# Kernel tuning notes

Hardware: AMD Instinct MI355X
Metric: run time of the kernel (lower is better)

Reference implementation:

```python
import jax, jax.numpy as jnp
import numpy as np

B, N, C, M = 1, 384, 128, 128
EPS = 1e-5

def _ln(x, g, b):
    mu = jnp.mean(x, axis=-1, keepdims=True)
    var = jnp.mean(jnp.square(x - mu), axis=-1, keepdims=True)
    return (x - mu) * jax.lax.rsqrt(var + EPS) * g + b

def setup_inputs() -> dict:
    key = jax.random.key(0)
    ks = jax.random.split(key, 12)
    s = 0.02
    return {
        "act": jax.random.normal(ks[0], (B, N, N, C), dtype=jnp.float32),
        "mask": jnp.ones((B, N, N), dtype=jnp.float32),
        "ln_g": jnp.ones((C,), jnp.float32), "ln_b": jnp.zeros((C,), jnp.float32),
        "Wl": s * jax.random.normal(ks[1], (C, M)), "bl": jnp.zeros((M,)),
        "Wr": s * jax.random.normal(ks[2], (C, M)), "br": jnp.zeros((M,)),
        "Wgl": s * jax.random.normal(ks[3], (C, M)), "bgl": jnp.zeros((M,)),
        "Wgr": s * jax.random.normal(ks[4], (C, M)), "bgr": jnp.zeros((M,)),
        "cg": jnp.ones((M,), jnp.float32), "cb": jnp.zeros((M,), jnp.float32),
        "Wo": s * jax.random.normal(ks[5], (M, C)), "bo": jnp.zeros((C,)),
        "Wg": s * jax.random.normal(ks[6], (C, C)), "bg": jnp.zeros((C,)),
    }

def reference(act, mask, ln_g, ln_b, Wl, bl, Wr, br, Wgl, bgl, Wgr, bgr, cg, cb, Wo, bo, Wg, bg):
    x = _ln(act, ln_g, ln_b)                      # [B,N,N,C]
    m = mask[..., None]                           # [B,N,N,1]
    left = m * (x @ Wl + bl) * jax.nn.sigmoid(x @ Wgl + bgl)   # [B,N,N,M]
    right = m * (x @ Wr + br) * jax.nn.sigmoid(x @ Wgr + bgr)  # [B,N,N,M]
    gate = jax.nn.sigmoid(x @ Wg + bg)            # [B,N,N,C]
    out = jnp.einsum('bikc,bjkc->bijc', left, right)  # triangle contraction over k
    out = _ln(out, cg, cb)
    out = (out @ Wo + bo) * gate
    return out
```

## Files before the change

kernel.cpp:

```cpp
#include <hip/hip_runtime.h>

#define EPS 1e-5f
#define NDIM 384
#define CDIM 128
#define NN (NDIM * NDIM)

typedef unsigned short ushort_t;
typedef __attribute__((ext_vector_type(8))) short short8;
typedef __attribute__((ext_vector_type(4))) float floatx4;
typedef __attribute__((ext_vector_type(4))) unsigned int uint4v;
typedef __attribute__((ext_vector_type(4))) float float4v;

static __device__ __forceinline__ ushort_t f2bf(float f) {
    unsigned int u = __builtin_bit_cast(unsigned int, f);
    u += 0x7FFFu + ((u >> 16) & 1u);
    return (ushort_t)(u >> 16);
}
static __device__ __forceinline__ float bf2f(ushort_t h) {
    unsigned int u = ((unsigned int)h) << 16;
    return __builtin_bit_cast(float, u);
}
static __device__ __forceinline__ float sigmoidf_(float x) {
    return 1.0f / (1.0f + __expf(-x));
}
static __device__ __forceinline__ floatx4 mfma16(short8 a, short8 b, floatx4 c) {
    return __builtin_amdgcn_mfma_f32_16x16x32_bf16(a, b, c, 0, 0, 0);
}

__global__ __launch_bounds__(256) void wconv6(
    const float* __restrict__ Wl, const float* __restrict__ Wr,
    const float* __restrict__ Wgl, const float* __restrict__ Wgr,
    const float* __restrict__ Wg, const float* __restrict__ Wo,
    ushort_t* __restrict__ wt)
{
    __shared__ float tile[128 * 132];
    const float* Ws[6] = {Wl, Wr, Wgl, Wgr, Wg, Wo};
    const float* W = Ws[blockIdx.x];
    ushort_t* dst = wt + blockIdx.x * 16384;
    const int t = threadIdx.x;
    for (int e = t; e < 16384; e += 256)
        tile[(e >> 7) * 132 + (e & 127)] = W[e];
    __syncthreads();
    for (int idx = t; idx < 16384; idx += 256) {
        int e = idx & 7, lane = (idx >> 3) & 63, kc = (idx >> 9) & 3, nt = idx >> 11;
        int n = nt * 16 + (lane & 15);
        int k = kc * 32 + (lane >> 4) * 8 + e;
        dst[idx] = f2bf(tile[k * 132 + n]);
    }
}

__global__ __launch_bounds__(256) void proj_kernel(
    const float* __restrict__ act, const float* __restrict__ mask,
    const float* __restrict__ ln_g, const float* __restrict__ ln_b,
    const float* __restrict__ bl, const float* __restrict__ bgl,
    const float* __restrict__ br, const float* __restrict__ bgr,
    const float* __restrict__ bg,
    const ushort_t* __restrict__ wt,
    ushort_t* __restrict__ leftT, ushort_t* __restrict__ rightT,
    ushort_t* __restrict__ gateO)
{
    __shared__ __align__(16) char smemA[32768];
    __shared__ ushort_t x_lds[64][136];
    __shared__ float mask_lds[64];
    float (*act_lds)[128] = (float (*)[128])smemA;
    ushort_t* st_lds = (ushort_t*)smemA;

    const int t = threadIdx.x;
    const int row0 = blockIdx.x * 64;
    const int i = row0 / NDIM;
    const int k0 = row0 % NDIM;
    const int wave = t >> 6;
    const int lane = t & 63;

#pragma unroll
    for (int q = 0; q < 8; ++q) {
        int e = (q * 256 + t) * 4;
        float4v v = *(const float4v*)(act + (size_t)row0 * CDIM + e);
        *(float4v*)&act_lds[e >> 7][e & 127] = v;
    }
    if (t < 64) mask_lds[t] = mask[row0 + t];
    __syncthreads();

    {
        const float g1 = ln_g[lane], g2 = ln_g[lane + 64];
        const float b1 = ln_b[lane], b2 = ln_b[lane + 64];
#pragma unroll
        for (int rr = 0; rr < 16; ++rr) {
            int r = wave * 16 + rr;
            float x1 = act_lds[r][lane], x2 = act_lds[r][lane + 64];
            float s = x1 + x2, s2 = x1 * x1 + x2 * x2;
#pragma unroll
            for (int off = 32; off >= 1; off >>= 1) {
                s  += __shfl_xor(s, off);
                s2 += __shfl_xor(s2, off);
            }
            float mu = s * (1.0f / 128.0f);
            float var = s2 * (1.0f / 128.0f) - mu * mu;
            float rstd = rsqrtf(var + EPS);
            x_lds[r][lane]      = f2bf((x1 - mu) * rstd * g1 + b1);
            x_lds[r][lane + 64] = f2bf((x2 - mu) * rstd * g2 + b2);
        }
    }
    __syncthreads();

    short8 afrag[4];
    {
        int r = wave * 16 + (lane & 15);
        int kb = (lane >> 4) * 8;
#pragma unroll
        for (int kc = 0; kc < 4; ++kc)
            afrag[kc] = *(const short8*)&x_lds[r][kc * 32 + kb];
    }

    const int n16 = lane & 15;

    auto do_pair = [&](const ushort_t* WtA, const ushort_t* WtB,
                       const float* __restrict__ bA, const float* __restrict__ bB) {
#pragma unroll
        for (int nt = 0; nt < 8; ++nt) {
            const int n = nt * 16 + n16;
            floatx4 accA = {0.f, 0.f, 0.f, 0.f};
            floatx4 accB = {0.f, 0.f, 0.f, 0.f};
#pragma unroll
            for (int kc = 0; kc < 4; ++kc) {
                short8 fbA = *(const short8*)&WtA[nt * 2048 + kc * 512 + lane * 8];
                accA = mfma16(afrag[kc], fbA, accA);
                short8 fbB = *(const short8*)&WtB[nt * 2048 + kc * 512 + lane * 8];
                accB = mfma16(afrag[kc], fbB, accB);
            }
            const float biasA = bA[n], biasB = bB[n];
#pragma unroll
            for (int reg = 0; reg < 4; ++reg) {
                int rloc = wave * 16 + (lane >> 4) * 4 + reg;
                float v = mask_lds[rloc] * (accA[reg] + biasA)
                                         * sigmoidf_(accB[reg] + biasB);
                st_lds[n * 72 + rloc] = f2bf(v);
            }
        }
    };

    auto flush_ck = [&](ushort_t* __restrict__ dst) {
        __syncthreads();
        int cc = t >> 1, kh = (t & 1) * 32;
        const uint4v* s = (const uint4v*)&st_lds[cc * 72 + kh];
        uint4v* d = (uint4v*)&dst[(size_t)cc * NN + i * NDIM + k0 + kh];
#pragma unroll
        for (int q = 0; q < 4; ++q) d[q] = s[q];
        __syncthreads();
    };

    do_pair(wt + 0 * 16384, wt + 2 * 16384, bl, bgl);
    flush_ck(leftT);
    do_pair(wt + 1 * 16384, wt + 3 * 16384, br, bgr);
    flush_ck(rightT);

    {
        const ushort_t* WtG = wt + 4 * 16384;
#pragma unroll
        for (int nt = 0; nt < 8; ++nt) {
            const int n = nt * 16 + n16;
            floatx4 acc = {0.f, 0.f, 0.f, 0.f};
#pragma unroll
            for (int kc = 0; kc < 4; ++kc) {
                short8 fb = *(const short8*)&WtG[nt * 2048 + kc * 512 + lane * 8];
                acc = mfma16(afrag[kc], fb, acc);
            }
            const float bias = bg[n];
#pragma unroll
            for (int reg = 0; reg < 4; ++reg) {
                int rloc = wave * 16 + (lane >> 4) * 4 + reg;
                st_lds[rloc * 128 + n] = f2bf(sigmoidf_(acc[reg] + bias));
            }
        }
        __syncthreads();
        int r = t >> 2, c0 = (t & 3) * 32;
        const uint4v* s = (const uint4v*)&st_lds[r * 128 + c0];
        uint4v* d = (uint4v*)&gateO[(size_t)(row0 + r) * CDIM + c0];
#pragma unroll
        for (int q = 0; q < 4; ++q) d[q] = s[q];
    }
}

__global__ __launch_bounds__(256) void tri_kernel(
    const ushort_t* __restrict__ leftT, const ushort_t* __restrict__ rightT,
    float* __restrict__ tri)
{
    __shared__ ushort_t Lt[128 * 72];
    __shared__ ushort_t Rt[128 * 72];
    const int t = threadIdx.x;
    const int bid0 = blockIdx.y * 9 + blockIdx.x;
    const int bid = (bid0 % 8) * 144 + (bid0 / 8);
    const int c = bid / 9;
    const int tile9 = bid % 9;
    const int it = tile9 / 3, jt = tile9 % 3;
    const int i0 = it * 128, j0 = jt * 128;
    const int wave = t >> 6, lane = t & 63;
    const int wi = (wave >> 1) * 64, wj = (wave & 1) * 64;

    const ushort_t* Lb = leftT + (size_t)c * NN + (size_t)i0 * NDIM;
    const ushort_t* Rb = rightT + (size_t)c * NN + (size_t)j0 * NDIM;

    floatx4 acc[4][4];
#pragma unroll
    for (int a = 0; a < 4; ++a)
#pragma unroll
        for (int b = 0; b < 4; ++b) acc[a][b] = (floatx4){0.f, 0.f, 0.f, 0.f};

    const int sr = t >> 1, skh = (t & 1) * 32;
    for (int kb = 0; kb < NDIM; kb += 64) {
        const uint4v* sL = (const uint4v*)&Lb[sr * NDIM + kb + skh];
        const uint4v* sR = (const uint4v*)&Rb[sr * NDIM + kb + skh];
        uint4v* dL = (uint4v*)&Lt[sr * 72 + skh];
        uint4v* dR = (uint4v*)&Rt[sr * 72 + skh];
#pragma unroll
        for (int q = 0; q < 4; ++q) { dL[q] = sL[q]; dR[q] = sR[q]; }
        __syncthreads();
#pragma unroll
        for (int kc = 0; kc < 2; ++kc) {
            const int kk = kc * 32 + (lane >> 4) * 8;
            short8 af[4], bfr[4];
#pragma unroll
            for (int mt = 0; mt < 4; ++mt)
                af[mt] = *(const short8*)&Lt[(wi + mt * 16 + (lane & 15)) * 72 + kk];
#pragma unroll
            for (int nt = 0; nt < 4; ++nt)
                bfr[nt] = *(const short8*)&Rt[(wj + nt * 16 + (lane & 15)) * 72 + kk];
#pragma unroll
            for (int mt = 0; mt < 4; ++mt)
#pragma unroll
                for (int nt = 0; nt < 4; ++nt)
                    acc[mt][nt] = mfma16(af[mt], bfr[nt], acc[mt][nt]);
        }
        __syncthreads();
    }

    float* outb = tri + (size_t)c * NN;
#pragma unroll
    for (int mt = 0; mt < 4; ++mt) {
#pragma unroll
        for (int reg = 0; reg < 4; ++reg) {
            int ii = i0 + wi + mt * 16 + (lane >> 4) * 4 + reg;
#pragma unroll
            for (int nt = 0; nt < 4; ++nt) {
                int jj = j0 + wj + nt * 16 + (lane & 15);
                outb[ii * NDIM + jj] = acc[mt][nt][reg];
            }
        }
    }
}

__global__ __launch_bounds__(256) void out_kernel(
    const float* __restrict__ tri, const float* __restrict__ cg,
    const float* __restrict__ cb,
    const ushort_t* __restrict__ wtO, const float* __restrict__ bo,
    const ushort_t* __restrict__ gate, float* __restrict__ outp)
{
    __shared__ __align__(16) float t_lds[64 * 132];
    __shared__ ushort_t x_lds[64][136];
    const int t = threadIdx.x;
    const int row0 = blockIdx.x * 64;
    const int i = row0 / NDIM, j0 = row0 % NDIM;
    const int wave = t >> 6, lane = t & 63;

    {
        const int c = t >> 1, jh = (t & 1) * 32;
        const float* src = tri + (size_t)c * NN + (size_t)i * NDIM + j0 + jh;
#pragma unroll
        for (int q = 0; q < 32; q += 4) {
            float4v v = *(const float4v*)(src + q);
            t_lds[(jh + q + 0) * 132 + c] = v.x;
            t_lds[(jh + q + 1) * 132 + c] = v.y;
            t_lds[(jh + q + 2) * 132 + c] = v.z;
            t_lds[(jh + q + 3) * 132 + c] = v.w;
        }
    }
    __syncthreads();

    {
        const float g1 = cg[lane], g2 = cg[lane + 64];
        const float b1 = cb[lane], b2 = cb[lane + 64];
#pragma unroll
        for (int rr = 0; rr < 16; ++rr) {
            int r = wave * 16 + rr;
            float x1 = t_lds[r * 132 + lane], x2 = t_lds[r * 132 + lane + 64];
            float s = x1 + x2, s2 = x1 * x1 + x2 * x2;
#pragma unroll
            for (int off = 32; off >= 1; off >>= 1) {
                s  += __shfl_xor(s, off);
                s2 += __shfl_xor(s2, off);
            }
            float mu = s * (1.0f / 128.0f);
            float var = s2 * (1.0f / 128.0f) - mu * mu;
            float rstd = rsqrtf(var + EPS);
            x_lds[r][lane]      = f2bf((x1 - mu) * rstd * g1 + b1);
            x_lds[r][lane + 64] = f2bf((x2 - mu) * rstd * g2 + b2);
        }
    }
    __syncthreads();

    short8 afrag[4];
    {
        int r = wave * 16 + (lane & 15);
        int kb = (lane >> 4) * 8;
#pragma unroll
        for (int kc = 0; kc < 4; ++kc)
            afrag[kc] = *(const short8*)&x_lds[r][kc * 32 + kb];
    }

    const int n16 = lane & 15;
#pragma unroll
    for (int nt = 0; nt < 8; ++nt) {
        const int n = nt * 16 + n16;
        floatx4 acc = {0.f, 0.f, 0.f, 0.f};
#pragma unroll
        for (int kc = 0; kc < 4; ++kc) {
            short8 fb = *(const short8*)&wtO[nt * 2048 + kc * 512 + lane * 8];
            acc = mfma16(afrag[kc], fb, acc);
        }
        const float bias = bo[n];
#pragma unroll
        for (int reg = 0; reg < 4; ++reg) {
            int rloc = wave * 16 + (lane >> 4) * 4 + reg;
            t_lds[rloc * 132 + n] = acc[reg] + bias;
        }
    }
    __syncthreads();

    {
        const int r = t >> 2, c0 = (t & 3) * 32;
        const uint4v* gv = (const uint4v*)&gate[(size_t)(row0 + r) * CDIM + c0];
        float4v* dst = (float4v*)&outp[(size_t)(row0 + r) * CDIM + c0];
#pragma unroll
        for (int q = 0; q < 4; ++q) {
            uint4v g8 = gv[q];
            float4v a = *(const float4v*)&t_lds[r * 132 + c0 + q * 8];
            float4v b = *(const float4v*)&t_lds[r * 132 + c0 + q * 8 + 4];
            a.x *= bf2f((ushort_t)(g8.x & 0xffff));
            a.y *= bf2f((ushort_t)(g8.x >> 16));
            a.z *= bf2f((ushort_t)(g8.y & 0xffff));
            a.w *= bf2f((ushort_t)(g8.y >> 16));
            b.x *= bf2f((ushort_t)(g8.z & 0xffff));
            b.y *= bf2f((ushort_t)(g8.z >> 16));
            b.z *= bf2f((ushort_t)(g8.w & 0xffff));
            b.w *= bf2f((ushort_t)(g8.w >> 16));
            dst[q * 2 + 0] = a;
            dst[q * 2 + 1] = b;
        }
    }
}

extern "C" void kernel_launch(void* const* d_in, const int* in_sizes, int n_in,
                              void* d_out, int out_size, void* d_ws, size_t ws_size,
                              hipStream_t stream)
{
    const float* act  = (const float*)d_in[0];
    const float* mask = (const float*)d_in[1];
    const float* ln_g = (const float*)d_in[2];
    const float* ln_b = (const float*)d_in[3];
    const float* Wl   = (const float*)d_in[4];
    const float* bl   = (const float*)d_in[5];
    const float* Wr   = (const float*)d_in[6];
    const float* br   = (const float*)d_in[7];
    const float* Wgl  = (const float*)d_in[8];
    const float* bgl  = (const float*)d_in[9];
    const float* Wgr  = (const float*)d_in[10];
    const float* bgr  = (const float*)d_in[11];
    const float* cg   = (const float*)d_in[12];
    const float* cb   = (const float*)d_in[13];
    const float* Wo   = (const float*)d_in[14];
    const float* bo   = (const float*)d_in[15];
    const float* Wg   = (const float*)d_in[16];
    const float* bg   = (const float*)d_in[17];
    float* outp = (float*)d_out;

    ushort_t* ws16  = (ushort_t*)d_ws;
    ushort_t* leftT  = ws16;
    ushort_t* rightT = ws16 + (size_t)CDIM * NN;
    ushort_t* gate   = ws16 + (size_t)2 * CDIM * NN;
    ushort_t* wt     = ws16 + (size_t)3 * CDIM * NN;
    float*    tri    = (float*)(ws16 + (size_t)3 * CDIM * NN + 6 * 16384);

    wconv6<<<6, 256, 0, stream>>>(Wl, Wr, Wgl, Wgr, Wg, Wo, wt);
    proj_kernel<<<NN / 64, 256, 0, stream>>>(act, mask, ln_g, ln_b,
                                             bl, bgl, br, bgr, bg,
                                             wt, leftT, rightT, gate);
    tri_kernel<<<dim3(9, 128), 256, 0, stream>>>(leftT, rightT, tri);
    out_kernel<<<NN / 64, 256, 0, stream>>>(tri, cg, cb, wt + 5 * 16384, bo,
                                            gate, outp);
}
```

Measured before the change: 342.4 us.

## Store triangle output in bf16 and read activations directly in projection

The triangle contraction result is now written as bf16 instead of fp32, which halves the intermediate tensor traffic between tri_kernel and out_kernel. out_kernel loads short8 vectors and converts them back to float in LDS. proj_kernel drops the 32KB LDS staging of act and reads rows straight from global memory, which shrinks LDS use and may raise occupancy, but the loads are less coalesced. Variance is clamped to non-negative. The bf16 intermediate costs precision before the LayerNorm.

Result: no change. 338.7 us (-1.1%).

```diff
diff --git a/kernel.cpp b/kernel.cpp
--- a/kernel.cpp
+++ b/kernel.cpp
@@ -59,11 +59,9 @@
     ushort_t* __restrict__ leftT, ushort_t* __restrict__ rightT,
     ushort_t* __restrict__ gateO)
 {
-    __shared__ __align__(16) char smemA[32768];
     __shared__ ushort_t x_lds[64][136];
+    __shared__ __align__(16) ushort_t st_lds[128 * 72];
     __shared__ float mask_lds[64];
-    float (*act_lds)[128] = (float (*)[128])smemA;
-    ushort_t* st_lds = (ushort_t*)smemA;
 
     const int t = threadIdx.x;
     const int row0 = blockIdx.x * 64;
@@ -72,14 +70,7 @@
     const int wave = t >> 6;
     const int lane = t & 63;
 
-#pragma unroll
-    for (int q = 0; q < 8; ++q) {
-        int e = (q * 256 + t) * 4;
-        float4v v = *(const float4v*)(act + (size_t)row0 * CDIM + e);
-        *(float4v*)&act_lds[e >> 7][e & 127] = v;
-    }
     if (t < 64) mask_lds[t] = mask[row0 + t];
-    __syncthreads();
 
     {
         const float g1 = ln_g[lane], g2 = ln_g[lane + 64];
@@ -87,7 +78,8 @@
 #pragma unroll
         for (int rr = 0; rr < 16; ++rr) {
             int r = wave * 16 + rr;
-            float x1 = act_lds[r][lane], x2 = act_lds[r][lane + 64];
+            const float* ar = act + (size_t)(row0 + r) * CDIM;
+            float x1 = ar[lane], x2 = ar[lane + 64];
             float s = x1 + x2, s2 = x1 * x1 + x2 * x2;
 #pragma unroll
             for (int off = 32; off >= 1; off >>= 1) {
@@ -96,7 +88,7 @@
             }
             float mu = s * (1.0f / 128.0f);
             float var = s2 * (1.0f / 128.0f) - mu * mu;
-            float rstd = rsqrtf(var + EPS);
+            float rstd = rsqrtf(fmaxf(var, 0.0f) + EPS);
             x_lds[r][lane]      = f2bf((x1 - mu) * rstd * g1 + b1);
             x_lds[r][lane + 64] = f2bf((x2 - mu) * rstd * g2 + b2);
         }
@@ -183,7 +175,7 @@
 
 __global__ __launch_bounds__(256) void tri_kernel(
     const ushort_t* __restrict__ leftT, const ushort_t* __restrict__ rightT,
-    float* __restrict__ tri)
+    ushort_t* __restrict__ tri)
 {
     __shared__ ushort_t Lt[128 * 72];
     __shared__ ushort_t Rt[128 * 72];
@@ -234,7 +226,7 @@
         __syncthreads();
     }
 
-    float* outb = tri + (size_t)c * NN;
+    ushort_t* outb = tri + (size_t)c * NN;
 #pragma unroll
     for (int mt = 0; mt < 4; ++mt) {
 #pragma unroll
@@ -243,14 +235,14 @@
 #pragma unroll
             for (int nt = 0; nt < 4; ++nt) {
                 int jj = j0 + wj + nt * 16 + (lane & 15);
-                outb[ii * NDIM + jj] = acc[mt][nt][reg];
+                outb[(size_t)ii * NDIM + jj] = f2bf(acc[mt][nt][reg]);
             }
         }
     }
 }
 
 __global__ __launch_bounds__(256) void out_kernel(
-    const float* __restrict__ tri, const float* __restrict__ cg,
+    const ushort_t* __restrict__ tri, const float* __restrict__ cg,
     const float* __restrict__ cb,
     const ushort_t* __restrict__ wtO, const float* __restrict__ bo,
     const ushort_t* __restrict__ gate, float* __restrict__ outp)
@@ -264,14 +256,13 @@
 
     {
         const int c = t >> 1, jh = (t & 1) * 32;
-        const float* src = tri + (size_t)c * NN + (size_t)i * NDIM + j0 + jh;
-#pragma unroll
-        for (int q = 0; q < 32; q += 4) {
-            float4v v = *(const float4v*)(src + q);
-            t_lds[(jh + q + 0) * 132 + c] = v.x;
-            t_lds[(jh + q + 1) * 132 + c] = v.y;
-            t_lds[(jh + q + 2) * 132 + c] = v.z;
-            t_lds[(jh + q + 3) * 132 + c] = v.w;
+        const ushort_t* src = tri + (size_t)c * NN + (size_t)i * NDIM + j0 + jh;
+#pragma unroll
+        for (int q = 0; q < 4; ++q) {
+            short8 v8 = *(const short8*)(src + q * 8);
+#pragma unroll
+            for (int e = 0; e < 8; ++e)
+                t_lds[(jh + q * 8 + e) * 132 + c] = bf2f((ushort_t)v8[e]);
         }
     }
     __syncthreads();
@@ -291,7 +282,7 @@
             }
             float mu = s * (1.0f / 128.0f);
             float var = s2 * (1.0f / 128.0f) - mu * mu;
-            float rstd = rsqrtf(var + EPS);
+            float rstd = rsqrtf(fmaxf(var, 0.0f) + EPS);
             x_lds[r][lane]      = f2bf((x1 - mu) * rstd * g1 + b1);
             x_lds[r][lane + 64] = f2bf((x2 - mu) * rstd * g2 + b2);
         }
@@ -373,18 +364,18 @@
     const float* bg   = (const float*)d_in[17];
     float* outp = (float*)d_out;
 
-    ushort_t* ws16  = (ushort_t*)d_ws;
+    ushort_t* ws16   = (ushort_t*)d_ws;
     ushort_t* leftT  = ws16;
     ushort_t* rightT = ws16 + (size_t)CDIM * NN;
     ushort_t* gate   = ws16 + (size_t)2 * CDIM * NN;
     ushort_t* wt     = ws16 + (size_t)3 * CDIM * NN;
-    float*    tri    = (float*)(ws16 + (size_t)3 * CDIM * NN + 6 * 16384);
+    ushort_t* triB   = ws16 + (size_t)3 * CDIM * NN + 6 * 16384;
 
     wconv6<<<6, 256, 0, stream>>>(Wl, Wr, Wgl, Wgr, Wg, Wo, wt);
     proj_kernel<<<NN / 64, 256, 0, stream>>>(act, mask, ln_g, ln_b,
                                              bl, bgl, br, bgr, bg,
                                              wt, leftT, rightT, gate);
-    tri_kernel<<<dim3(9, 128), 256, 0, stream>>>(leftT, rightT, tri);
-    out_kernel<<<NN / 64, 256, 0, stream>>>(tri, cg, cb, wt + 5 * 16384, bo,
+    tri_kernel<<<dim3(9, 128), 256, 0, stream>>>(leftT, rightT, triB);
+    out_kernel<<<NN / 64, 256, 0, stream>>>(triB, cg, cb, wt + 5 * 16384, bo,
                                             gate, outp);
 }
```
